# Kernel tuning notes

Measured on AMD Instinct MI355X. Metric: run time of the kernel, lower is better.

The kernel has to match this reference:

```python
import jax, jax.numpy as jnp
import numpy as np
from jax import lax

NUM_CLASSES = 5
NUM_TASKS = 20
CONV_CHANS = [(64, 3), (64, 64), (128, 64), (128, 128), (256, 128), (256, 256)]  # (out, in)


def setup_inputs() -> dict:
    key = jax.random.key(0)
    ks = jax.random.split(key, 16)
    B = 512
    x = jax.random.normal(ks[0], (B, 3, 32, 32), dtype=jnp.float32)
    tid = jax.random.randint(ks[1], (B,), 0, NUM_TASKS)
    inp = {"x": x, "tid": tid}
    for i, (oc, ic) in enumerate(CONV_CHANS):
        fan_in = ic * 9
        inp[f"w{i}"] = jax.random.normal(ks[2 + 2 * i], (oc, ic, 3, 3), dtype=jnp.float32) * np.float32((2.0 / fan_in) ** 0.5)
        inp[f"b{i}"] = jnp.zeros((oc,), dtype=jnp.float32)
    inp["cw"] = jax.random.normal(ks[14], (NUM_CLASSES * NUM_TASKS, 4096), dtype=jnp.float32) * np.float32(4096 ** -0.5)
    inp["cb"] = jnp.zeros((NUM_CLASSES * NUM_TASKS,), dtype=jnp.float32)
    return inp


def _conv_relu(x, w, b):
    y = lax.conv_general_dilated(x, w, window_strides=(1, 1), padding='SAME',
                                 dimension_numbers=('NCHW', 'OIHW', 'NCHW'))
    return jax.nn.relu(y + b[None, :, None, None])


def _maxpool2(x):
    return lax.reduce_window(x, -jnp.inf, lax.max, (1, 1, 2, 2), (1, 1, 2, 2), 'VALID')


def _forward(x, tid, ws, bs, cw, cb):
    # VGG cfg [64,64,'M',128,128,'M',256,256,'M']
    h = _conv_relu(x, ws[0], bs[0])
    h = _conv_relu(h, ws[1], bs[1])
    h = _maxpool2(h)
    h = _conv_relu(h, ws[2], bs[2])
    h = _conv_relu(h, ws[3], bs[3])
    h = _maxpool2(h)
    h = _conv_relu(h, ws[4], bs[4])
    h = _conv_relu(h, ws[5], bs[5])
    h = _maxpool2(h)                      # [B, 256, 4, 4]
    feat = h.reshape(h.shape[0], -1)      # [B, 4096], matches torch NCHW flatten
    # Batched task-indexed classifier: gather each sample's 5-row weight block.
    w_sel = cw.reshape(NUM_TASKS, NUM_CLASSES, 4096)[tid]   # [B, 5, 4096]
    b_sel = cb.reshape(NUM_TASKS, NUM_CLASSES)[tid]         # [B, 5]
    return jnp.einsum('bcd,bd->bc', w_sel, feat) + b_sel


def reference(x, tid, w0, b0, w1, b1, w2, b2, w3, b3, w4, b4, w5, b5, cw, cb):
    ws = (w0, w1, w2, w3, w4, w5)
    bs = (b0, b1, b2, b3, b4, b5)
    return _forward(x, tid, ws, bs, cw, cb)
```

## Files before the change

kernel.cpp:

```cpp
#include <hip/hip_runtime.h>


typedef __attribute__((ext_vector_type(8))) short short8;
typedef __attribute__((ext_vector_type(4))) float floatx4;
typedef unsigned int uint;
typedef unsigned short ushort;

__device__ __forceinline__ ushort f2bf(float f) {
    uint u = __float_as_uint(f);
    return (ushort)((u + 0x7fffu + ((u >> 16) & 1u)) >> 16);
}
__device__ __forceinline__ float bf2f(ushort h) {
    return __uint_as_float(((uint)h) << 16);
}

typedef const __attribute__((address_space(1))) unsigned int* gas_ptr;
typedef __attribute__((address_space(3))) unsigned int* las_ptr;
__device__ __forceinline__ void gload_lds16(const void* g, void* l) {
    __builtin_amdgcn_global_load_lds((gas_ptr)g, (las_ptr)l, 16, 0, 0);
}

__device__ __forceinline__ void wlin_one(
    const float* __restrict__ src, short* __restrict__ dst, int OC, int IC, int o)
{
    int j    = o & 7;
    int lane = (o >> 3) & 63;
    int r    = o >> 9;
    int G16  = OC >> 4;
    int g    = r % G16;  r /= G16;
    int kk   = r % 9;
    int icb  = r / 9;
    int oc = g * 16 + (lane & 15);
    int ic = icb * 32 + (lane >> 4) * 8 + j;
    dst[o] = (short)f2bf(src[((long)oc * IC + ic) * 9 + kk]);
}

#define N_W0 2048
#define N_W1 36864
#define N_W2 73728
#define N_W3 147456
#define N_W4 294912
#define N_W5 589824
#define N_WT_TOTAL (N_W0 + N_W1 + N_W2 + N_W3 + N_W4 + N_W5)

__global__ __launch_bounds__(256) void wtransform_all(
    const float* __restrict__ w0, const float* __restrict__ w1,
    const float* __restrict__ w2, const float* __restrict__ w3,
    const float* __restrict__ w4, const float* __restrict__ w5,
    short* __restrict__ wt0, short* __restrict__ wts1, short* __restrict__ wts2,
    short* __restrict__ wts3, short* __restrict__ wts4, short* __restrict__ wts5,
    short* __restrict__ zp)
{
    if (blockIdx.x == 0 && threadIdx.x < 32) zp[threadIdx.x] = 0;
    int idx = blockIdx.x * 256 + threadIdx.x;
    if (idx < N_W0) {
        int oc = idx >> 5, k = idx & 31;
        wt0[idx] = (k < 27) ? (short)f2bf(w0[oc * 27 + k]) : (short)0;
        return;
    }
    idx -= N_W0;
    if (idx < N_W1) { wlin_one(w1, wts1, 64, 64, idx); return; }
    idx -= N_W1;
    if (idx < N_W2) { wlin_one(w2, wts2, 128, 64, idx); return; }
    idx -= N_W2;
    if (idx < N_W3) { wlin_one(w3, wts3, 128, 128, idx); return; }
    idx -= N_W3;
    if (idx < N_W4) { wlin_one(w4, wts4, 256, 128, idx); return; }
    idx -= N_W4;
    wlin_one(w5, wts5, 256, 256, idx);
}

__global__ __launch_bounds__(256, 2) void conv0_mfma(
    const float* __restrict__ x, const short* __restrict__ wT0,
    const float* __restrict__ b0, ushort* __restrict__ out)
{
    __shared__ float  s_x[3 * 18 * 34];
    __shared__ ushort s_b[4 * 512 * 8];

    const int tid  = threadIdx.x;
    const int wv   = tid >> 6;
    const int lane = tid & 63;
    const int quad = lane >> 4;
    const int l16  = lane & 15;
    const int b    = blockIdx.x >> 1;
    const int r0   = (blockIdx.x & 1) * 16;

    for (int idx = tid; idx < 3 * 18 * 34; idx += 256) {
        int c   = idx / 612;
        int rem = idx - c * 612;
        int ry  = rem / 34, rx = rem - ry * 34;
        int gy  = r0 + ry - 1, gx = rx - 1;
        float v = 0.f;
        if (gy >= 0 && gy < 32 && gx >= 0 && gx < 32)
            v = x[(((long)b * 3 + c) * 32 + gy) * 32 + gx];
        s_x[idx] = v;
    }
    __syncthreads();

#pragma unroll
    for (int rep = 0; rep < 2; ++rep) {
        int pxl = rep * 256 + tid;
        int py = pxl >> 5, px = pxl & 31;
        ushort v[32];
#pragma unroll
        for (int c = 0; c < 3; ++c)
#pragma unroll
            for (int ky = 0; ky < 3; ++ky)
#pragma unroll
                for (int kx = 0; kx < 3; ++kx)
                    v[c * 9 + ky * 3 + kx] = f2bf(s_x[c * 612 + (py + ky) * 34 + (px + kx)]);
#pragma unroll
        for (int k = 27; k < 32; ++k) v[k] = 0;
#pragma unroll
        for (int q = 0; q < 4; ++q)
            *(uint4*)(&s_b[(q * 512 + pxl) * 8]) = *(const uint4*)(v + q * 8);
    }
    __syncthreads();

    floatx4 acc[4][8];
#pragma unroll
    for (int i = 0; i < 4; ++i)
#pragma unroll
        for (int t = 0; t < 8; ++t) acc[i][t] = (floatx4)0.f;

    short8 afr[4];
#pragma unroll
    for (int i = 0; i < 4; ++i)
        afr[i] = *(const short8*)(wT0 + (i * 16 + l16) * 32 + quad * 8);
#pragma unroll
    for (int t = 0; t < 8; ++t) {
        int pxl = wv * 128 + t * 16 + l16;
        short8 bfr = *(const short8*)(&s_b[(quad * 512 + pxl) * 8]);
#pragma unroll
        for (int i = 0; i < 4; ++i)
            acc[i][t] = __builtin_amdgcn_mfma_f32_16x16x32_bf16(afr[i], bfr, acc[i][t], 0, 0, 0);
    }

#pragma unroll
    for (int i = 0; i < 4; ++i) {
        int oc0 = i * 16 + quad * 4;
        float4 bv = *(const float4*)(b0 + oc0);
#pragma unroll
        for (int t = 0; t < 8; ++t) {
            int pxl = wv * 128 + t * 16 + l16;
            int py = pxl >> 5, px = pxl & 31;
            long dst = ((((long)b * 8 + (oc0 >> 3)) * 32 + r0 + py) * 32 + px) * 8 + (oc0 & 7);
            float v0 = acc[i][t][0] + bv.x;
            float v1 = acc[i][t][1] + bv.y;
            float v2 = acc[i][t][2] + bv.z;
            float v3 = acc[i][t][3] + bv.w;
            ushort o[4];
            o[0] = f2bf(v0 > 0.f ? v0 : 0.f);
            o[1] = f2bf(v1 > 0.f ? v1 : 0.f);
            o[2] = f2bf(v2 > 0.f ? v2 : 0.f);
            o[3] = f2bf(v3 > 0.f ? v3 : 0.f);
            *(uint2*)(out + dst) = *(uint2*)o;
        }
    }
}

template<int IC, int OC, int H, int W, int ROWS, int OCGROUPS, bool POOL>
__global__ __launch_bounds__(256, 3) void conv_so(
    const ushort* __restrict__ act_in,
    const short*  __restrict__ wTs,
    const float*  __restrict__ bias,
    ushort* __restrict__ act_out,
    const ushort* __restrict__ zp)
{
    constexpr int WPAD  = W + 2;
    constexpr int RPAD  = ROWS + 2;
    constexpr int UNITS = RPAD * WPAD;
    constexpr int SEGS  = H / ROWS;
    constexpr int C8I   = IC / 8;
    constexpr int G16   = OC / 16;
    constexpr int NICB  = IC / 32;
    constexpr int C8O   = OC / 8;
    constexpr int TMAX  = NICB * 9;
    constexpr int NSTG  = UNITS * C8I;

    __shared__ ushort s_act[NSTG * 8];

    const int tid  = threadIdx.x;
    const int wv   = tid >> 6;
    const int lane = tid & 63;
    const int quad = lane >> 4;
    const int l16  = lane & 15;

    const int b   = blockIdx.x / SEGS;
    const int seg = blockIdx.x - b * SEGS;
    const int r0  = seg * ROWS;
    const int ocg = wv % OCGROUPS;
    const int pxg = wv / OCGROUPS;

    for (int c = tid; c < NSTG; c += 256) {
        int sub  = c / UNITS;
        int unit = c - sub * UNITS;
        int ry   = unit / WPAD, cx = unit - ry * WPAD;
        int gy   = r0 + ry - 1, gx = cx - 1;
        const ushort* src = zp;
        if ((unsigned)gy < (unsigned)H && (unsigned)gx < (unsigned)W)
            src = act_in + ((((long)b * C8I + sub) * H + gy) * W + gx) * 8;
        gload_lds16(src, &s_act[(size_t)(c - lane) * 8]);
    }
    __syncthreads();

    floatx4 acc[4][4];
#pragma unroll
    for (int i = 0; i < 4; ++i)
#pragma unroll
        for (int t = 0; t < 4; ++t) acc[i][t] = (floatx4)0.f;

    int bbase[4];
#pragma unroll
    for (int t = 0; t < 4; ++t) {
        int pxl = pxg * 64 + t * 16 + l16;
        int py  = pxl / W, px = pxl - py * W;
        bbase[t] = (py * WPAD + px) * 8;
    }

    const short8* wb = (const short8*)wTs;
    const int  wbase = (ocg * 4) * 64 + lane;
    const long WSTEP = (long)G16 * 64;

    short8 wpipe[3][4];
#pragma unroll
    for (int d = 0; d < 3; ++d)
#pragma unroll
        for (int i = 0; i < 4; ++i)
            wpipe[d][i] = wb[(long)d * WSTEP + wbase + i * 64];

    int tl = 0;
    for (int icb = 0; icb < NICB; ++icb) {
#pragma unroll
        for (int kk = 0; kk < 9; ++kk) {
            const int ky = kk / 3, kx = kk - ky * 3;
            const int koff = ((icb * 4 + quad) * UNITS + ky * WPAD + kx) * 8;
            short8 bfr[4];
#pragma unroll
            for (int t = 0; t < 4; ++t)
                bfr[t] = *(const short8*)(&s_act[bbase[t] + koff]);
            const int slot = kk % 3;
#pragma unroll
            for (int i = 0; i < 4; ++i)
#pragma unroll
                for (int t = 0; t < 4; ++t)
                    acc[i][t] = __builtin_amdgcn_mfma_f32_16x16x32_bf16(
                        wpipe[slot][i], bfr[t], acc[i][t], 0, 0, 0);
            int tn = tl + 3;
            if (tn >= TMAX) tn = 0;
#pragma unroll
            for (int i = 0; i < 4; ++i)
                wpipe[slot][i] = wb[(long)tn * WSTEP + wbase + i * 64];
            ++tl;
        }
    }

    if constexpr (!POOL) {
#pragma unroll
        for (int i = 0; i < 4; ++i) {
            int oc0 = ocg * 64 + i * 16 + quad * 4;
            float4 bv = *(const float4*)(bias + oc0);
#pragma unroll
            for (int t = 0; t < 4; ++t) {
                int pxl = pxg * 64 + t * 16 + l16;
                int py  = pxl / W, px = pxl - py * W;
                long dst = ((((long)b * C8O + (oc0 >> 3)) * H + r0 + py) * W + px) * 8 + (oc0 & 7);
                float v0 = acc[i][t][0] + bv.x;
                float v1 = acc[i][t][1] + bv.y;
                float v2 = acc[i][t][2] + bv.z;
                float v3 = acc[i][t][3] + bv.w;
                ushort o[4];
                o[0] = f2bf(v0 > 0.f ? v0 : 0.f);
                o[1] = f2bf(v1 > 0.f ? v1 : 0.f);
                o[2] = f2bf(v2 > 0.f ? v2 : 0.f);
                o[3] = f2bf(v3 > 0.f ? v3 : 0.f);
                *(uint2*)(act_out + dst) = *(uint2*)o;
            }
        }
    } else {
        __syncthreads();
        ushort* s_pool = s_act;
        constexpr int PSTR = OC + 8;
        static_assert(ROWS * W * PSTR <= NSTG * 8, "pool scratch fits");
#pragma unroll
        for (int i = 0; i < 4; ++i) {
            int oc0 = ocg * 64 + i * 16 + quad * 4;
            float4 bv = *(const float4*)(bias + oc0);
#pragma unroll
            for (int t = 0; t < 4; ++t) {
                int pxl = pxg * 64 + t * 16 + l16;
                float v0 = acc[i][t][0] + bv.x;
                float v1 = acc[i][t][1] + bv.y;
                float v2 = acc[i][t][2] + bv.z;
                float v3 = acc[i][t][3] + bv.w;
                ushort o[4];
                o[0] = f2bf(v0 > 0.f ? v0 : 0.f);
                o[1] = f2bf(v1 > 0.f ? v1 : 0.f);
                o[2] = f2bf(v2 > 0.f ? v2 : 0.f);
                o[3] = f2bf(v3 > 0.f ? v3 : 0.f);
                *(uint2*)(&s_pool[pxl * PSTR + oc0]) = *(uint2*)o;
            }
        }
        __syncthreads();
        constexpr int PH = ROWS / 2, PW = W / 2, HOT = H / 2;
        const int pr0 = r0 / 2;
        for (int u = tid; u < PH * PW * C8O; u += 256) {
            int c8 = u % C8O;
            int pp = u / C8O;
            int xo = pp % PW, yo = pp / PW;
            const ushort* p00 = &s_pool[((2 * yo) * W + 2 * xo) * PSTR + c8 * 8];
            uint4 q0 = *(const uint4*)(p00);
            uint4 q1 = *(const uint4*)(p00 + PSTR);
            uint4 q2 = *(const uint4*)(p00 + W * PSTR);
            uint4 q3 = *(const uint4*)(p00 + W * PSTR + PSTR);
            const ushort* a0 = (const ushort*)&q0;
            const ushort* a1 = (const ushort*)&q1;
            const ushort* a2 = (const ushort*)&q2;
            const ushort* a3 = (const ushort*)&q3;
            ushort r[8];
#pragma unroll
            for (int j = 0; j < 8; ++j) {
                ushort m0 = a0[j] > a1[j] ? a0[j] : a1[j];
                ushort m1 = a2[j] > a3[j] ? a2[j] : a3[j];
                r[j] = m0 > m1 ? m0 : m1;
            }
            long dst = ((((long)b * C8O + c8) * HOT + pr0 + yo) * PW + xo) * 8;
            *(uint4*)(act_out + dst) = *(uint4*)r;
        }
    }
}

template<int IC, int OC, bool POOL>
__global__ __launch_bounds__(512, 2) void conv_so2(
    const ushort* __restrict__ act_in,
    const short*  __restrict__ wTs,
    const float*  __restrict__ bias,
    ushort* __restrict__ act_out,
    const ushort* __restrict__ zp)
{
    constexpr int H = 8, W = 8;
    constexpr int WPAD  = 10;
    constexpr int UNITS = 10 * 10;
    constexpr int C8I   = IC / 8;
    constexpr int G16   = OC / 16;
    constexpr int NICB  = IC / 32;
    constexpr int C8O   = OC / 8;
    constexpr int TMAX  = NICB * 9;
    constexpr int NSTG  = UNITS * C8I;

    __shared__ ushort s_act[2 * NSTG * 8];

    const int tid  = threadIdx.x;
    const int wv   = tid >> 6;
    const int lane = tid & 63;
    const int quad = lane >> 4;
    const int l16  = lane & 15;

    const int ocg  = wv & 3;
    const int img2 = wv >> 2;
    const long b0i = (long)blockIdx.x * 2;

    for (int c = tid; c < 2 * NSTG; c += 512) {
        int img  = c / NSTG;
        int cc   = c - img * NSTG;
        int sub  = cc / UNITS;
        int unit = cc - sub * UNITS;
        int ry   = unit / WPAD, cx = unit - ry * WPAD;
        int gy   = ry - 1, gx = cx - 1;
        const ushort* src = zp;
        if ((unsigned)gy < (unsigned)H && (unsigned)gx < (unsigned)W)
            src = act_in + ((((b0i + img) * C8I + sub) * H + gy) * W + gx) * 8;
        gload_lds16(src, &s_act[(size_t)(c - lane) * 8]);
    }
    __syncthreads();

    floatx4 acc[4][4];
#pragma unroll
    for (int i = 0; i < 4; ++i)
#pragma unroll
        for (int t = 0; t < 4; ++t) acc[i][t] = (floatx4)0.f;

    int bbase[4];
#pragma unroll
    for (int t = 0; t < 4; ++t) {
        int pxl = t * 16 + l16;
        int py  = pxl >> 3, px = pxl & 7;
        bbase[t] = (py * WPAD + px) * 8 + img2 * NSTG * 8;
    }

    const short8* wb = (const short8*)wTs;
    const int  wbase = (ocg * 4) * 64 + lane;
    const long WSTEP = (long)G16 * 64;

    short8 wpipe[3][4];
#pragma unroll
    for (int d = 0; d < 3; ++d)
#pragma unroll
        for (int i = 0; i < 4; ++i)
            wpipe[d][i] = wb[(long)d * WSTEP + wbase + i * 64];

    int tl = 0;
    for (int icb = 0; icb < NICB; ++icb) {
#pragma unroll
        for (int kk = 0; kk < 9; ++kk) {
            const int ky = kk / 3, kx = kk - ky * 3;
            const int koff = ((icb * 4 + quad) * UNITS + ky * WPAD + kx) * 8;
            short8 bfr[4];
#pragma unroll
            for (int t = 0; t < 4; ++t)
                bfr[t] = *(const short8*)(&s_act[bbase[t] + koff]);
            const int slot = kk % 3;
#pragma unroll
            for (int i = 0; i < 4; ++i)
#pragma unroll
                for (int t = 0; t < 4; ++t)
                    acc[i][t] = __builtin_amdgcn_mfma_f32_16x16x32_bf16(
                        wpipe[slot][i], bfr[t], acc[i][t], 0, 0, 0);
            int tn = tl + 3;
            if (tn >= TMAX) tn = 0;
#pragma unroll
            for (int i = 0; i < 4; ++i)
                wpipe[slot][i] = wb[(long)tn * WSTEP + wbase + i * 64];
            ++tl;
        }
    }

    const long b = b0i + img2;
    if constexpr (!POOL) {
#pragma unroll
        for (int i = 0; i < 4; ++i) {
            int oc0 = ocg * 64 + i * 16 + quad * 4;
            float4 bv = *(const float4*)(bias + oc0);
#pragma unroll
            for (int t = 0; t < 4; ++t) {
                int pxl = t * 16 + l16;
                int py  = pxl >> 3, px = pxl & 7;
                long dst = (((b * C8O + (oc0 >> 3)) * H + py) * W + px) * 8 + (oc0 & 7);
                float v0 = acc[i][t][0] + bv.x;
                float v1 = acc[i][t][1] + bv.y;
                float v2 = acc[i][t][2] + bv.z;
                float v3 = acc[i][t][3] + bv.w;
                ushort o[4];
                o[0] = f2bf(v0 > 0.f ? v0 : 0.f);
                o[1] = f2bf(v1 > 0.f ? v1 : 0.f);
                o[2] = f2bf(v2 > 0.f ? v2 : 0.f);
                o[3] = f2bf(v3 > 0.f ? v3 : 0.f);
                *(uint2*)(act_out + dst) = *(uint2*)o;
            }
        }
    } else {
        __syncthreads();
        ushort* s_pool = s_act;
        constexpr int PSTR = OC + 8;
        static_assert(H * W * PSTR <= NSTG * 8, "pool scratch fits per image");
        ushort* my_pool = s_pool + (size_t)img2 * NSTG * 8;
#pragma unroll
        for (int i = 0; i < 4; ++i) {
            int oc0 = ocg * 64 + i * 16 + quad * 4;
            float4 bv = *(const float4*)(bias + oc0);
#pragma unroll
            for (int t = 0; t < 4; ++t) {
                int pxl = t * 16 + l16;
                float v0 = acc[i][t][0] + bv.x;
                float v1 = acc[i][t][1] + bv.y;
                float v2 = acc[i][t][2] + bv.z;
                float v3 = acc[i][t][3] + bv.w;
                ushort o[4];
                o[0] = f2bf(v0 > 0.f ? v0 : 0.f);
                o[1] = f2bf(v1 > 0.f ? v1 : 0.f);
                o[2] = f2bf(v2 > 0.f ? v2 : 0.f);
                o[3] = f2bf(v3 > 0.f ? v3 : 0.f);
                *(uint2*)(&my_pool[pxl * PSTR + oc0]) = *(uint2*)o;
            }
        }
        __syncthreads();
        constexpr int PH = 4, PW = 4, HOT = 4;
        for (int u = tid; u < 2 * PH * PW * C8O; u += 512) {
            int img = u / (PH * PW * C8O);
            int uu  = u - img * (PH * PW * C8O);
            int c8 = uu % C8O;
            int pp = uu / C8O;
            int xo = pp % PW, yo = pp / PW;
            const ushort* p00 = &s_pool[(size_t)img * NSTG * 8 + ((2 * yo) * W + 2 * xo) * PSTR + c8 * 8];
            uint4 q0 = *(const uint4*)(p00);
            uint4 q1 = *(const uint4*)(p00 + PSTR);
            uint4 q2 = *(const uint4*)(p00 + W * PSTR);
            uint4 q3 = *(const uint4*)(p00 + W * PSTR + PSTR);
            const ushort* a0 = (const ushort*)&q0;
            const ushort* a1 = (const ushort*)&q1;
            const ushort* a2 = (const ushort*)&q2;
            const ushort* a3 = (const ushort*)&q3;
            ushort r[8];
#pragma unroll
            for (int j = 0; j < 8; ++j) {
                ushort m0 = a0[j] > a1[j] ? a0[j] : a1[j];
                ushort m1 = a2[j] > a3[j] ? a2[j] : a3[j];
                r[j] = m0 > m1 ? m0 : m1;
            }
            long dst = ((((b0i + img) * C8O + c8) * HOT + yo) * PW + xo) * 8;
            *(uint4*)(act_out + dst) = *(uint4*)r;
        }
    }
}

__global__ __launch_bounds__(256) void classifier_k(
    const ushort* __restrict__ feat, const int* __restrict__ tids,
    const float* __restrict__ cw, const float* __restrict__ cb,
    float* __restrict__ out, int B)
{
    int g = blockIdx.x * 256 + threadIdx.x;
    int wid = g >> 6, lane = g & 63;
    if (wid >= B * 5) return;
    int b = wid / 5, c = wid - b * 5;
    int t = tids[b];
    const float* wrow = cw + (long)(t * 5 + c) * 4096;
    const ushort* f = feat + (long)b * 4096;
    float s = 0.f;
#pragma unroll 4
    for (int d = lane; d < 4096; d += 64) {
        int fidx = (((d >> 7) * 16) + (d & 15)) * 8 + ((d >> 4) & 7);
        s += wrow[d] * bf2f(f[fidx]);
    }
#pragma unroll
    for (int off = 32; off > 0; off >>= 1) s += __shfl_down(s, off, 64);
    if (lane == 0) out[wid] = s + cb[t * 5 + c];
}

extern "C" void kernel_launch(void* const* d_in, const int* in_sizes, int n_in,
                              void* d_out, int out_size, void* d_ws, size_t ws_size,
                              hipStream_t stream)
{
    const float* x   = (const float*)d_in[0];
    const int*   tid = (const int*)d_in[1];
    const float* w0 = (const float*)d_in[2];  const float* b0 = (const float*)d_in[3];
    const float* w1 = (const float*)d_in[4];  const float* b1 = (const float*)d_in[5];
    const float* w2 = (const float*)d_in[6];  const float* b2 = (const float*)d_in[7];
    const float* w3 = (const float*)d_in[8];  const float* b3 = (const float*)d_in[9];
    const float* w4 = (const float*)d_in[10]; const float* b4 = (const float*)d_in[11];
    const float* w5 = (const float*)d_in[12]; const float* b5 = (const float*)d_in[13];
    const float* cw = (const float*)d_in[14];
    const float* cb = (const float*)d_in[15];
    float* outp = (float*)d_out;

    const int B = in_sizes[0] / (3 * 32 * 32);

    short* wt0  = (short*)d_ws;
    short* wts1 = wt0 + N_W0;
    short* wts2 = wts1 + N_W1;
    short* wts3 = wts2 + N_W2;
    short* wts4 = wts3 + N_W3;
    short* wts5 = wts4 + N_W4;
    short* zp   = wts5 + N_W5;
    const size_t WT_HW = (size_t)N_WT_TOTAL + 32;
    const size_t fixed_bytes = WT_HW * 2;

    int Bc = B;
    while (Bc > 2 && fixed_bytes + (size_t)Bc * 2 * 65536 * 2 > ws_size) Bc >>= 1;
    if (Bc < 2) Bc = 2;

    ushort* bufA = (ushort*)((short*)d_ws + WT_HW);
    ushort* bufB = bufA + (size_t)Bc * 65536;

    wtransform_all<<<(N_WT_TOTAL + 255) / 256, 256, 0, stream>>>(
        w0, w1, w2, w3, w4, w5, wt0, wts1, wts2, wts3, wts4, wts5, zp);

    for (int cb0 = 0; cb0 < B; cb0 += Bc) {
        const float* xc = x + (size_t)cb0 * 3 * 32 * 32;
        const int* tidc = tid + cb0;
        float* outc = outp + (size_t)cb0 * 5;

        conv0_mfma<<<Bc * 2, 256, 0, stream>>>(xc, wt0, b0, bufA);
        conv_so<64, 64, 32, 32, 8, 1, true><<<Bc * 4, 256, 0, stream>>>(bufA, wts1, b1, bufB, (ushort*)zp);
        conv_so<64, 128, 16, 16, 8, 2, false><<<Bc * 2, 256, 0, stream>>>(bufB, wts2, b2, bufA, (ushort*)zp);
        conv_so<128, 128, 16, 16, 8, 2, true><<<Bc * 2, 256, 0, stream>>>(bufA, wts3, b3, bufB, (ushort*)zp);
        conv_so2<128, 256, false><<<Bc / 2, 512, 0, stream>>>(bufB, wts4, b4, bufA, (ushort*)zp);
        conv_so2<256, 256, true><<<Bc / 2, 512, 0, stream>>>(bufA, wts5, b5, bufB, (ushort*)zp);
        classifier_k<<<(Bc * 5 * 64 + 255) / 256, 256, 0, stream>>>(bufB, tidc, cw, cb, outc, Bc);
    }
}
```

Baseline: 315.5 us.

## Fuse classifier into last conv, share weights across two images, pad LDS

The 8x8 conv kernels now run 256 threads per block, and each wave computes both images of the pair, so every weight fragment loaded from global memory feeds twice as many MFMAs. The separate classifier kernel is removed. The last conv block writes pooled features to shared memory and computes the task-selected dot products against a bf16 copy of the classifier weights produced in the weight-transform kernel. LDS channel strides are padded by two units to reduce bank conflicts in all conv_so kernels. In exchange, the doubled accumulators raise register pressure and occupancy drops (launch bounds 256,1), and classifier weights become bf16, which adds rounding error.

```diff
diff --git a/kernel.cpp b/kernel.cpp
--- a/kernel.cpp
+++ b/kernel.cpp
@@ -41,15 +41,18 @@
 #define N_W3 147456
 #define N_W4 294912
 #define N_W5 589824
+#define N_CWB (100 * 4096)
 #define N_WT_TOTAL (N_W0 + N_W1 + N_W2 + N_W3 + N_W4 + N_W5)
+#define N_ALL (N_WT_TOTAL + N_CWB)
 
 __global__ __launch_bounds__(256) void wtransform_all(
     const float* __restrict__ w0, const float* __restrict__ w1,
     const float* __restrict__ w2, const float* __restrict__ w3,
     const float* __restrict__ w4, const float* __restrict__ w5,
+    const float* __restrict__ cw,
     short* __restrict__ wt0, short* __restrict__ wts1, short* __restrict__ wts2,
     short* __restrict__ wts3, short* __restrict__ wts4, short* __restrict__ wts5,
-    short* __restrict__ zp)
+    short* __restrict__ zp, short* __restrict__ cwb)
 {
     if (blockIdx.x == 0 && threadIdx.x < 32) zp[threadIdx.x] = 0;
     int idx = blockIdx.x * 256 + threadIdx.x;
@@ -67,7 +70,9 @@
     idx -= N_W3;
     if (idx < N_W4) { wlin_one(w4, wts4, 256, 128, idx); return; }
     idx -= N_W4;
-    wlin_one(w5, wts5, 256, 256, idx);
+    if (idx < N_W5) { wlin_one(w5, wts5, 256, 256, idx); return; }
+    idx -= N_W5;
+    if (idx < N_CWB) cwb[idx] = (short)f2bf(cw[idx]);
 }
 
 __global__ __launch_bounds__(256, 2) void conv0_mfma(
@@ -170,13 +175,14 @@
     constexpr int WPAD  = W + 2;
     constexpr int RPAD  = ROWS + 2;
     constexpr int UNITS = RPAD * WPAD;
+    constexpr int UNITSP = UNITS + 2;
     constexpr int SEGS  = H / ROWS;
     constexpr int C8I   = IC / 8;
     constexpr int G16   = OC / 16;
     constexpr int NICB  = IC / 32;
     constexpr int C8O   = OC / 8;
     constexpr int TMAX  = NICB * 9;
-    constexpr int NSTG  = UNITS * C8I;
+    constexpr int NSTG  = UNITSP * C8I;
 
     __shared__ ushort s_act[NSTG * 8];
 
@@ -193,12 +199,12 @@
     const int pxg = wv / OCGROUPS;
 
     for (int c = tid; c < NSTG; c += 256) {
-        int sub  = c / UNITS;
-        int unit = c - sub * UNITS;
+        int sub  = c / UNITSP;
+        int unit = c - sub * UNITSP;
         int ry   = unit / WPAD, cx = unit - ry * WPAD;
         int gy   = r0 + ry - 1, gx = cx - 1;
         const ushort* src = zp;
-        if ((unsigned)gy < (unsigned)H && (unsigned)gx < (unsigned)W)
+        if (unit < UNITS && (unsigned)gy < (unsigned)H && (unsigned)gx < (unsigned)W)
             src = act_in + ((((long)b * C8I + sub) * H + gy) * W + gx) * 8;
         gload_lds16(src, &s_act[(size_t)(c - lane) * 8]);
     }
@@ -234,7 +240,7 @@
 #pragma unroll
         for (int kk = 0; kk < 9; ++kk) {
             const int ky = kk / 3, kx = kk - ky * 3;
-            const int koff = ((icb * 4 + quad) * UNITS + ky * WPAD + kx) * 8;
+            const int koff = ((icb * 4 + quad) * UNITSP + ky * WPAD + kx) * 8;
             short8 bfr[4];
 #pragma unroll
             for (int t = 0; t < 4; ++t)
@@ -330,23 +336,28 @@
     }
 }
 
-template<int IC, int OC, bool POOL>
-__global__ __launch_bounds__(512, 2) void conv_so2(
+template<int IC, int OC, bool POOL, bool CLS>
+__global__ __launch_bounds__(256, 1) void conv_so2i(
     const ushort* __restrict__ act_in,
     const short*  __restrict__ wTs,
     const float*  __restrict__ bias,
     ushort* __restrict__ act_out,
-    const ushort* __restrict__ zp)
+    const ushort* __restrict__ zp,
+    const int*   __restrict__ tids,
+    const short* __restrict__ cwb,
+    const float* __restrict__ cbv,
+    float*       __restrict__ outp)
 {
     constexpr int H = 8, W = 8;
     constexpr int WPAD  = 10;
-    constexpr int UNITS = 10 * 10;
+    constexpr int UNITS = 100;
+    constexpr int UNITSP = 102;
     constexpr int C8I   = IC / 8;
     constexpr int G16   = OC / 16;
     constexpr int NICB  = IC / 32;
     constexpr int C8O   = OC / 8;
     constexpr int TMAX  = NICB * 9;
-    constexpr int NSTG  = UNITS * C8I;
+    constexpr int NSTG  = UNITSP * C8I;
 
     __shared__ ushort s_act[2 * NSTG * 8];
 
@@ -355,38 +366,40 @@
     const int lane = tid & 63;
     const int quad = lane >> 4;
     const int l16  = lane & 15;
-
-    const int ocg  = wv & 3;
-    const int img2 = wv >> 2;
+    const int ocg  = wv;
     const long b0i = (long)blockIdx.x * 2;
 
-    for (int c = tid; c < 2 * NSTG; c += 512) {
+    for (int c = tid; c < 2 * NSTG; c += 256) {
         int img  = c / NSTG;
         int cc   = c - img * NSTG;
-        int sub  = cc / UNITS;
-        int unit = cc - sub * UNITS;
+        int sub  = cc / UNITSP;
+        int unit = cc - sub * UNITSP;
         int ry   = unit / WPAD, cx = unit - ry * WPAD;
         int gy   = ry - 1, gx = cx - 1;
         const ushort* src = zp;
-        if ((unsigned)gy < (unsigned)H && (unsigned)gx < (unsigned)W)
+        if (unit < UNITS && (unsigned)gy < (unsigned)H && (unsigned)gx < (unsigned)W)
             src = act_in + ((((b0i + img) * C8I + sub) * H + gy) * W + gx) * 8;
         gload_lds16(src, &s_act[(size_t)(c - lane) * 8]);
     }
     __syncthreads();
 
-    floatx4 acc[4][4];
+    floatx4 acc[4][2][4];
 #pragma unroll
     for (int i = 0; i < 4; ++i)
 #pragma unroll
-        for (int t = 0; t < 4; ++t) acc[i][t] = (floatx4)0.f;
-
-    int bbase[4];
-#pragma unroll
-    for (int t = 0; t < 4; ++t) {
-        int pxl = t * 16 + l16;
-        int py  = pxl >> 3, px = pxl & 7;
-        bbase[t] = (py * WPAD + px) * 8 + img2 * NSTG * 8;
-    }
+        for (int g = 0; g < 2; ++g)
+#pragma unroll
+            for (int t = 0; t < 4; ++t) acc[i][g][t] = (floatx4)0.f;
+
+    int bbase[2][4];
+#pragma unroll
+    for (int g = 0; g < 2; ++g)
+#pragma unroll
+        for (int t = 0; t < 4; ++t) {
+            int pxl = t * 16 + l16;
+            int py  = pxl >> 3, px = pxl & 7;
+            bbase[g][t] = (py * WPAD + px) * 8 + g * NSTG * 8;
+        }
 
     const short8* wb = (const short8*)wTs;
     const int  wbase = (ocg * 4) * 64 + lane;
@@ -404,18 +417,22 @@
 #pragma unroll
         for (int kk = 0; kk < 9; ++kk) {
             const int ky = kk / 3, kx = kk - ky * 3;
-            const int koff = ((icb * 4 + quad) * UNITS + ky * WPAD + kx) * 8;
-            short8 bfr[4];
-#pragma unroll
-            for (int t = 0; t < 4; ++t)
-                bfr[t] = *(const short8*)(&s_act[bbase[t] + koff]);
+            const int koff = ((icb * 4 + quad) * UNITSP + ky * WPAD + kx) * 8;
+            short8 bfr[2][4];
+#pragma unroll
+            for (int g = 0; g < 2; ++g)
+#pragma unroll
+                for (int t = 0; t < 4; ++t)
+                    bfr[g][t] = *(const short8*)(&s_act[bbase[g][t] + koff]);
             const int slot = kk % 3;
 #pragma unroll
             for (int i = 0; i < 4; ++i)
 #pragma unroll
-                for (int t = 0; t < 4; ++t)
-                    acc[i][t] = __builtin_amdgcn_mfma_f32_16x16x32_bf16(
-                        wpipe[slot][i], bfr[t], acc[i][t], 0, 0, 0);
+                for (int g = 0; g < 2; ++g)
+#pragma unroll
+                    for (int t = 0; t < 4; ++t)
+                        acc[i][g][t] = __builtin_amdgcn_mfma_f32_16x16x32_bf16(
+                            wpipe[slot][i], bfr[g][t], acc[i][g][t], 0, 0, 0);
             int tn = tl + 3;
             if (tn >= TMAX) tn = 0;
 #pragma unroll
@@ -425,57 +442,61 @@
         }
     }
 
-    const long b = b0i + img2;
     if constexpr (!POOL) {
 #pragma unroll
         for (int i = 0; i < 4; ++i) {
             int oc0 = ocg * 64 + i * 16 + quad * 4;
             float4 bv = *(const float4*)(bias + oc0);
 #pragma unroll
-            for (int t = 0; t < 4; ++t) {
-                int pxl = t * 16 + l16;
-                int py  = pxl >> 3, px = pxl & 7;
-                long dst = (((b * C8O + (oc0 >> 3)) * H + py) * W + px) * 8 + (oc0 & 7);
-                float v0 = acc[i][t][0] + bv.x;
-                float v1 = acc[i][t][1] + bv.y;
-                float v2 = acc[i][t][2] + bv.z;
-                float v3 = acc[i][t][3] + bv.w;
-                ushort o[4];
-                o[0] = f2bf(v0 > 0.f ? v0 : 0.f);
-                o[1] = f2bf(v1 > 0.f ? v1 : 0.f);
-                o[2] = f2bf(v2 > 0.f ? v2 : 0.f);
-                o[3] = f2bf(v3 > 0.f ? v3 : 0.f);
-                *(uint2*)(act_out + dst) = *(uint2*)o;
-            }
+            for (int g = 0; g < 2; ++g)
+#pragma unroll
+                for (int t = 0; t < 4; ++t) {
+                    int pxl = t * 16 + l16;
+                    int py  = pxl >> 3, px = pxl & 7;
+                    long dst = ((((b0i + g) * C8O + (oc0 >> 3)) * H + py) * W + px) * 8 + (oc0 & 7);
+                    float v0 = acc[i][g][t][0] + bv.x;
+                    float v1 = acc[i][g][t][1] + bv.y;
+                    float v2 = acc[i][g][t][2] + bv.z;
+                    float v3 = acc[i][g][t][3] + bv.w;
+                    ushort o[4];
+                    o[0] = f2bf(v0 > 0.f ? v0 : 0.f);
+                    o[1] = f2bf(v1 > 0.f ? v1 : 0.f);
+                    o[2] = f2bf(v2 > 0.f ? v2 : 0.f);
+                    o[3] = f2bf(v3 > 0.f ? v3 : 0.f);
+                    *(uint2*)(act_out + dst) = *(uint2*)o;
+                }
         }
     } else {
         __syncthreads();
         ushort* s_pool = s_act;
         constexpr int PSTR = OC + 8;
         static_assert(H * W * PSTR <= NSTG * 8, "pool scratch fits per image");
-        ushort* my_pool = s_pool + (size_t)img2 * NSTG * 8;
+        static_assert(!CLS || (2 * NSTG * 8 - 8192 >= NSTG * 8 + H * W * PSTR), "s_feat fits");
 #pragma unroll
         for (int i = 0; i < 4; ++i) {
             int oc0 = ocg * 64 + i * 16 + quad * 4;
             float4 bv = *(const float4*)(bias + oc0);
 #pragma unroll
-            for (int t = 0; t < 4; ++t) {
-                int pxl = t * 16 + l16;
-                float v0 = acc[i][t][0] + bv.x;
-                float v1 = acc[i][t][1] + bv.y;
-                float v2 = acc[i][t][2] + bv.z;
-                float v3 = acc[i][t][3] + bv.w;
-                ushort o[4];
-                o[0] = f2bf(v0 > 0.f ? v0 : 0.f);
-                o[1] = f2bf(v1 > 0.f ? v1 : 0.f);
-                o[2] = f2bf(v2 > 0.f ? v2 : 0.f);
-                o[3] = f2bf(v3 > 0.f ? v3 : 0.f);
-                *(uint2*)(&my_pool[pxl * PSTR + oc0]) = *(uint2*)o;
-            }
+            for (int g = 0; g < 2; ++g)
+#pragma unroll
+                for (int t = 0; t < 4; ++t) {
+                    int pxl = t * 16 + l16;
+                    float v0 = acc[i][g][t][0] + bv.x;
+                    float v1 = acc[i][g][t][1] + bv.y;
+                    float v2 = acc[i][g][t][2] + bv.z;
+                    float v3 = acc[i][g][t][3] + bv.w;
+                    ushort o[4];
+                    o[0] = f2bf(v0 > 0.f ? v0 : 0.f);
+                    o[1] = f2bf(v1 > 0.f ? v1 : 0.f);
+                    o[2] = f2bf(v2 > 0.f ? v2 : 0.f);
+                    o[3] = f2bf(v3 > 0.f ? v3 : 0.f);
+                    *(uint2*)(&s_pool[(size_t)g * NSTG * 8 + pxl * PSTR + oc0]) = *(uint2*)o;
+                }
         }
         __syncthreads();
         constexpr int PH = 4, PW = 4, HOT = 4;
-        for (int u = tid; u < 2 * PH * PW * C8O; u += 512) {
+        ushort* s_feat = s_act + (2 * NSTG * 8 - 8192);
+        for (int u = tid; u < 2 * PH * PW * C8O; u += 256) {
             int img = u / (PH * PW * C8O);
             int uu  = u - img * (PH * PW * C8O);
             int c8 = uu % C8O;
@@ -497,33 +518,38 @@
                 ushort m1 = a2[j] > a3[j] ? a2[j] : a3[j];
                 r[j] = m0 > m1 ? m0 : m1;
             }
-            long dst = ((((b0i + img) * C8O + c8) * HOT + yo) * PW + xo) * 8;
-            *(uint4*)(act_out + dst) = *(uint4*)r;
-        }
-    }
-}
-
-__global__ __launch_bounds__(256) void classifier_k(
-    const ushort* __restrict__ feat, const int* __restrict__ tids,
-    const float* __restrict__ cw, const float* __restrict__ cb,
-    float* __restrict__ out, int B)
-{
-    int g = blockIdx.x * 256 + threadIdx.x;
-    int wid = g >> 6, lane = g & 63;
-    if (wid >= B * 5) return;
-    int b = wid / 5, c = wid - b * 5;
-    int t = tids[b];
-    const float* wrow = cw + (long)(t * 5 + c) * 4096;
-    const ushort* f = feat + (long)b * 4096;
-    float s = 0.f;
-#pragma unroll 4
-    for (int d = lane; d < 4096; d += 64) {
-        int fidx = (((d >> 7) * 16) + (d & 15)) * 8 + ((d >> 4) & 7);
-        s += wrow[d] * bf2f(f[fidx]);
-    }
-#pragma unroll
-    for (int off = 32; off > 0; off >>= 1) s += __shfl_down(s, off, 64);
-    if (lane == 0) out[wid] = s + cb[t * 5 + c];
+            if constexpr (CLS) {
+#pragma unroll
+                for (int j = 0; j < 8; ++j)
+                    s_feat[img * 4096 + (c8 * 8 + j) * 16 + pp] = r[j];
+            } else {
+                long dst = ((((b0i + img) * C8O + c8) * HOT + yo) * PW + xo) * 8;
+                *(uint4*)(act_out + dst) = *(uint4*)r;
+            }
+        }
+        if constexpr (CLS) {
+            __syncthreads();
+            const int t0 = tids[b0i], t1 = tids[b0i + 1];
+            for (int u = wv; u < 10; u += 4) {
+                int img = u & 1, c = u >> 1;
+                int t = img ? t1 : t0;
+                const short* wrow = cwb + (long)(t * 5 + c) * 4096;
+                const ushort* f = s_feat + img * 4096;
+                float s = 0.f;
+#pragma unroll
+                for (int j = 0; j < 8; ++j) {
+                    short8 wv8 = *(const short8*)(wrow + lane * 8 + 512 * j);
+                    short8 fv8 = *(const short8*)(f + lane * 8 + 512 * j);
+#pragma unroll
+                    for (int e = 0; e < 8; ++e)
+                        s += bf2f((ushort)wv8[e]) * bf2f((ushort)fv8[e]);
+                }
+#pragma unroll
+                for (int off = 32; off > 0; off >>= 1) s += __shfl_down(s, off, 64);
+                if (lane == 0) outp[(b0i + img) * 5 + c] = s + cbv[t * 5 + c];
+            }
+        }
+    }
 }
 
 extern "C" void kernel_launch(void* const* d_in, const int* in_sizes, int n_in,
@@ -551,7 +577,8 @@
     short* wts4 = wts3 + N_W3;
     short* wts5 = wts4 + N_W4;
     short* zp   = wts5 + N_W5;
-    const size_t WT_HW = (size_t)N_WT_TOTAL + 32;
+    short* cwb  = zp + 32;
+    const size_t WT_HW = (size_t)N_WT_TOTAL + 32 + N_CWB;
     const size_t fixed_bytes = WT_HW * 2;
 
     int Bc = B;
@@ -561,8 +588,9 @@
     ushort* bufA = (ushort*)((short*)d_ws + WT_HW);
     ushort* bufB = bufA + (size_t)Bc * 65536;
 
-    wtransform_all<<<(N_WT_TOTAL + 255) / 256, 256, 0, stream>>>(
-        w0, w1, w2, w3, w4, w5, wt0, wts1, wts2, wts3, wts4, wts5, zp);
+    wtransform_all<<<(N_ALL + 255) / 256, 256, 0, stream>>>(
+        w0, w1, w2, w3, w4, w5, cw,
+        wt0, wts1, wts2, wts3, wts4, wts5, zp, cwb);
 
     for (int cb0 = 0; cb0 < B; cb0 += Bc) {
         const float* xc = x + (size_t)cb0 * 3 * 32 * 32;
@@ -570,11 +598,15 @@
         float* outc = outp + (size_t)cb0 * 5;
 
         conv0_mfma<<<Bc * 2, 256, 0, stream>>>(xc, wt0, b0, bufA);
-        conv_so<64, 64, 32, 32, 8, 1, true><<<Bc * 4, 256, 0, stream>>>(bufA, wts1, b1, bufB, (ushort*)zp);
-        conv_so<64, 128, 16, 16, 8, 2, false><<<Bc * 2, 256, 0, stream>>>(bufB, wts2, b2, bufA, (ushort*)zp);
-        conv_so<128, 128, 16, 16, 8, 2, true><<<Bc * 2, 256, 0, stream>>>(bufA, wts3, b3, bufB, (ushort*)zp);
-        conv_so2<128, 256, false><<<Bc / 2, 512, 0, stream>>>(bufB, wts4, b4, bufA, (ushort*)zp);
-        conv_so2<256, 256, true><<<Bc / 2, 512, 0, stream>>>(bufA, wts5, b5, bufB, (ushort*)zp);
-        classifier_k<<<(Bc * 5 * 64 + 255) / 256, 256, 0, stream>>>(bufB, tidc, cw, cb, outc, Bc);
-    }
-}
+        conv_so<64, 64, 32, 32, 8, 1, true><<<Bc * 4, 256, 0, stream>>>(
+            bufA, wts1, b1, bufB, (ushort*)zp);
+        conv_so<64, 128, 16, 16, 8, 2, false><<<Bc * 2, 256, 0, stream>>>(
+            bufB, wts2, b2, bufA, (ushort*)zp);
+        conv_so<128, 128, 16, 16, 8, 2, true><<<Bc * 2, 256, 0, stream>>>(
+            bufA, wts3, b3, bufB, (ushort*)zp);
+        conv_so2i<128, 256, false, false><<<Bc / 2, 256, 0, stream>>>(
+            bufB, wts4, b4, bufA, (ushort*)zp, nullptr, nullptr, nullptr, nullptr);
+        conv_so2i<256, 256, true, true><<<Bc / 2, 256, 0, stream>>>(
+            bufA, wts5, b5, bufB, (ushort*)zp, tidc, cwb, cb, outc);
+    }
+}
```

Measured after the change: 318.9 us. Within noise of the previous version (+1.1%).
